# Performance work log

Measured on AMD Instinct MI355X. Metric: run time of the kernel, lower is better.

## Reference

```python
import jax, jax.numpy as jnp
import numpy as np

IN_DIM = 128
OUT_DIM = 128
NUM_INTERVALS = 8
SPLINE_ORDER = 3
BATCH = 1024


def make_grids():
    # domain [-1, 1] for every (in, out) pair, extended by spline_order knots each side
    step = 2.0 / NUM_INTERVALS
    G = NUM_INTERVALS + 2 * SPLINE_ORDER + 1
    g = (-1.0 - SPLINE_ORDER * step) + jnp.arange(G, dtype=jnp.float32) * step  # [G]
    return jnp.broadcast_to(g, (IN_DIM, OUT_DIM, G))


def setup_inputs() -> dict:
    key = jax.random.key(0)
    k1, k2, k3 = jax.random.split(key, 3)
    x = jax.random.normal(k1, (BATCH, IN_DIM), dtype=jnp.float32)
    n_cp = NUM_INTERVALS + SPLINE_ORDER
    control_points = 0.1 * jax.random.normal(k2, (IN_DIM, OUT_DIM, n_cp), dtype=jnp.float32)
    scaling_factors = np.sqrt(2.0 / OUT_DIM).astype(np.float32) * jax.random.normal(
        k3, (IN_DIM, OUT_DIM), dtype=jnp.float32)
    grids = make_grids()
    return {"x": x, "control_points": control_points,
            "scaling_factors": scaling_factors, "grids": grids}


def bspline_bases(x, grids, k):
    # Bottom-up Cox-de-Boor DP (identical recurrence to the naive top-down version).
    # x: [B, in], grids: [in, out, G] -> returns all degree-k bases [B, in, out, G-1-k]
    ex = x[:, :, None, None]          # [B, in, 1, 1]
    t = grids[None]                   # [1, in, out, G]
    B = ((t[..., :-1] <= ex) & (ex < t[..., 1:])).astype(x.dtype)  # degree 0
    for d in range(1, k + 1):
        tl  = t[..., : -(d + 1)]      # t[i]
        tr  = t[..., d:-1]            # t[i+d]
        tl1 = t[..., 1:-d]            # t[i+1]
        tr1 = t[..., d + 1:]          # t[i+d+1]
        B = (ex - tl) / (tr - tl) * B[..., :-1] + (tr1 - ex) / (tr1 - tl1) * B[..., 1:]
    return B


def reference(x, control_points, scaling_factors, grids):
    Bk = bspline_bases(x, grids, SPLINE_ORDER)                 # [B, in, out, n_cp]
    spline = jnp.einsum('biog,iog->bio', Bk, control_points)    # [B, in, out]
    res = scaling_factors[None] * (jax.nn.silu(x)[:, :, None] + spline)
    return jnp.sum(res, axis=1).astype(jnp.float32)             # [B, out]
```

## Files before the change

### kernel.cpp

```cpp
#include <hip/hip_runtime.h>
#include <math.h>


#define IN_DIM   128
#define OUT_DIM  128
#define NCP      11
#define GK       15
#define FS       12
#define KTOT     (IN_DIM * FS)
#define BT       8
#define OT       32
#define VO       4
#define KSP      32
#define NJ       12
#define THREADS  256
#define RPAD     260

__global__ __launch_bounds__(256)
void kan_prep(const float* __restrict__ CP,
              const float* __restrict__ SF,
              float* __restrict__ W)
{
    const int p = blockIdx.x * 256 + threadIdx.x;
    const int i = p >> 7;
    const int o = p & (OUT_DIM - 1);
    const float s = SF[p];
    const float* cp = CP + p * NCP;
    const int kb = i * FS;
    #pragma unroll
    for (int g = 0; g < NCP; ++g)
        W[(kb + g) * OUT_DIM + o] = s * cp[g];
    W[(kb + NCP) * OUT_DIM + o] = s;
}

__global__ __launch_bounds__(THREADS, 2)
void kan_main(const float* __restrict__ X,
              const float* __restrict__ GR,
              const float* __restrict__ W,
              float* __restrict__ OUT)
{
    __shared__ float F[BT * KTOT];

    const int tid = threadIdx.x;
    const int b0  = blockIdx.x * BT;
    const int o0  = blockIdx.y * OT;

    const float t0 = GR[0];
    const float h  = GR[1] - t0;
    const float r1 = 1.0f / h;
    const float r2 = 1.0f / (2.0f * h);
    const float r3 = 1.0f / (3.0f * h);
    float kn[GK];
    #pragma unroll
    for (int j = 0; j < GK; ++j) kn[j] = t0 + (float)j * h;

    #pragma unroll
    for (int kq = 0; kq < (BT * IN_DIM) / THREADS; ++kq) {
        const int p = tid + kq * THREADS;
        const int r = p >> 7;
        const int i = p & (IN_DIM - 1);

        const float x = X[(b0 + r) * IN_DIM + i];

        float b[GK - 1];
        #pragma unroll
        for (int j = 0; j < GK - 1; ++j)
            b[j] = (kn[j] <= x && x < kn[j + 1]) ? 1.0f : 0.0f;
        #pragma unroll
        for (int j = 0; j < GK - 2; ++j)
            b[j] = ((x - kn[j]) * b[j] + (kn[j + 2] - x) * b[j + 1]) * r1;
        #pragma unroll
        for (int j = 0; j < GK - 3; ++j)
            b[j] = ((x - kn[j]) * b[j] + (kn[j + 3] - x) * b[j + 1]) * r2;
        #pragma unroll
        for (int j = 0; j < GK - 4; ++j)
            b[j] = ((x - kn[j]) * b[j] + (kn[j + 4] - x) * b[j + 1]) * r3;

        const float silu = x / (1.0f + __expf(-x));

        float* f = &F[p * FS];
        *(float4*)(f + 0) = make_float4(b[0], b[1], b[2], b[3]);
        *(float4*)(f + 4) = make_float4(b[4], b[5], b[6], b[7]);
        *(float4*)(f + 8) = make_float4(b[8], b[9], b[10], silu);
    }
    __syncthreads();

    const int ol = tid & (OT / VO - 1);
    const int ks = tid >> 3;
    const int o4 = o0 + VO * ol;

    float acc[BT][VO];
    #pragma unroll
    for (int r = 0; r < BT; ++r)
        #pragma unroll
        for (int v = 0; v < VO; ++v) acc[r][v] = 0.0f;

    #pragma unroll
    for (int j = 0; j < NJ; ++j) {
        const int kg = 4 * (ks + KSP * j);

        float4 w0 = *(const float4*)&W[(kg + 0) * OUT_DIM + o4];
        float4 w1 = *(const float4*)&W[(kg + 1) * OUT_DIM + o4];
        float4 w2 = *(const float4*)&W[(kg + 2) * OUT_DIM + o4];
        float4 w3 = *(const float4*)&W[(kg + 3) * OUT_DIM + o4];

        #pragma unroll
        for (int r = 0; r < BT; ++r) {
            const float4 f = *(const float4*)&F[r * KTOT + kg];
            acc[r][0] = fmaf(f.x, w0.x, acc[r][0]);
            acc[r][1] = fmaf(f.x, w0.y, acc[r][1]);
            acc[r][2] = fmaf(f.x, w0.z, acc[r][2]);
            acc[r][3] = fmaf(f.x, w0.w, acc[r][3]);
            acc[r][0] = fmaf(f.y, w1.x, acc[r][0]);
            acc[r][1] = fmaf(f.y, w1.y, acc[r][1]);
            acc[r][2] = fmaf(f.y, w1.z, acc[r][2]);
            acc[r][3] = fmaf(f.y, w1.w, acc[r][3]);
            acc[r][0] = fmaf(f.z, w2.x, acc[r][0]);
            acc[r][1] = fmaf(f.z, w2.y, acc[r][1]);
            acc[r][2] = fmaf(f.z, w2.z, acc[r][2]);
            acc[r][3] = fmaf(f.z, w2.w, acc[r][3]);
            acc[r][0] = fmaf(f.w, w3.x, acc[r][0]);
            acc[r][1] = fmaf(f.w, w3.y, acc[r][1]);
            acc[r][2] = fmaf(f.w, w3.z, acc[r][2]);
            acc[r][3] = fmaf(f.w, w3.w, acc[r][3]);
        }
    }

    __syncthreads();
    float* red = F;
    #pragma unroll
    for (int r = 0; r < BT; ++r)
        *(float4*)&red[ks * RPAD + r * OT + VO * ol] =
            make_float4(acc[r][0], acc[r][1], acc[r][2], acc[r][3]);
    __syncthreads();

    {
        const int r  = tid >> 5;
        const int oc = tid & 31;
        float v = 0.0f;
        #pragma unroll
        for (int q = 0; q < KSP; ++q)
            v += red[q * RPAD + r * OT + oc];
        OUT[(b0 + r) * OUT_DIM + o0 + oc] = v;
    }
}

extern "C" void kernel_launch(void* const* d_in, const int* in_sizes, int n_in,
                              void* d_out, int out_size, void* d_ws, size_t ws_size,
                              hipStream_t stream) {
    const float* x  = (const float*)d_in[0];
    const float* cp = (const float*)d_in[1];
    const float* sf = (const float*)d_in[2];
    const float* gr = (const float*)d_in[3];
    float* out = (float*)d_out;
    float* W   = (float*)d_ws;

    const int batch = in_sizes[0] / IN_DIM;

    kan_prep<<<(IN_DIM * OUT_DIM) / 256, 256, 0, stream>>>(cp, sf, W);
    dim3 grid(batch / BT, OUT_DIM / OT);
    kan_main<<<grid, THREADS, 0, stream>>>(x, gr, W, out);
}
```

Baseline: 69.31 us.

## Fuse weight prep into main kernel, reading control points and scales directly

```diff
diff --git a/kernel.cpp b/kernel.cpp
--- a/kernel.cpp
+++ b/kernel.cpp
@@ -12,32 +12,23 @@
 #define OT       32
 #define VO       4
 #define KSP      32
-#define NJ       12
+#define NI       (IN_DIM / KSP)
 #define THREADS  256
 #define RPAD     260
 
-__global__ __launch_bounds__(256)
-void kan_prep(const float* __restrict__ CP,
-              const float* __restrict__ SF,
-              float* __restrict__ W)
-{
-    const int p = blockIdx.x * 256 + threadIdx.x;
-    const int i = p >> 7;
-    const int o = p & (OUT_DIM - 1);
-    const float s = SF[p];
-    const float* cp = CP + p * NCP;
-    const int kb = i * FS;
-    #pragma unroll
-    for (int g = 0; g < NCP; ++g)
-        W[(kb + g) * OUT_DIM + o] = s * cp[g];
-    W[(kb + NCP) * OUT_DIM + o] = s;
+typedef float f4v __attribute__((ext_vector_type(4)));
+typedef f4v uf4 __attribute__((aligned(4)));
+
+__device__ __forceinline__ f4v ld4u(const float* __restrict__ p) {
+    return *(const uf4*)p;
 }
 
 __global__ __launch_bounds__(THREADS, 2)
-void kan_main(const float* __restrict__ X,
-              const float* __restrict__ GR,
-              const float* __restrict__ W,
-              float* __restrict__ OUT)
+void kan_fused(const float* __restrict__ X,
+               const float* __restrict__ CP,
+               const float* __restrict__ SF,
+               const float* __restrict__ GR,
+               float* __restrict__ OUT)
 {
     __shared__ float F[BT * KTOT];
 
@@ -96,33 +87,51 @@
         for (int v = 0; v < VO; ++v) acc[r][v] = 0.0f;
 
     #pragma unroll
-    for (int j = 0; j < NJ; ++j) {
-        const int kg = 4 * (ks + KSP * j);
+    for (int jj = 0; jj < NI; ++jj) {
+        const int i = ks + KSP * jj;
+        const float4 sf4 = *(const float4*)&SF[i * OUT_DIM + o4];
+        const float* cb = CP + (i * OUT_DIM + o4) * NCP;
 
-        float4 w0 = *(const float4*)&W[(kg + 0) * OUT_DIM + o4];
-        float4 w1 = *(const float4*)&W[(kg + 1) * OUT_DIM + o4];
-        float4 w2 = *(const float4*)&W[(kg + 2) * OUT_DIM + o4];
-        float4 w3 = *(const float4*)&W[(kg + 3) * OUT_DIM + o4];
+        f4v c[VO][3];
+        #pragma unroll
+        for (int v = 0; v < VO; ++v) {
+            const float s = (v == 0) ? sf4.x : (v == 1) ? sf4.y
+                          : (v == 2) ? sf4.z : sf4.w;
+            const float* cv = cb + v * NCP;
+            f4v a0 = ld4u(cv + 0);
+            f4v a1 = ld4u(cv + 4);
+            f4v a2 = ld4u(cv + 7);
+            c[v][0] = s * a0;
+            c[v][1] = s * a1;
+            c[v][2].x = s;
+            c[v][2].y = s * a2.y;
+            c[v][2].z = s * a2.z;
+            c[v][2].w = s * a2.w;
+        }
 
+        const int fb = i * FS;
         #pragma unroll
         for (int r = 0; r < BT; ++r) {
-            const float4 f = *(const float4*)&F[r * KTOT + kg];
-            acc[r][0] = fmaf(f.x, w0.x, acc[r][0]);
-            acc[r][1] = fmaf(f.x, w0.y, acc[r][1]);
-            acc[r][2] = fmaf(f.x, w0.z, acc[r][2]);
-            acc[r][3] = fmaf(f.x, w0.w, acc[r][3]);
-            acc[r][0] = fmaf(f.y, w1.x, acc[r][0]);
-            acc[r][1] = fmaf(f.y, w1.y, acc[r][1]);
-            acc[r][2] = fmaf(f.y, w1.z, acc[r][2]);
-            acc[r][3] = fmaf(f.y, w1.w, acc[r][3]);
-            acc[r][0] = fmaf(f.z, w2.x, acc[r][0]);
-            acc[r][1] = fmaf(f.z, w2.y, acc[r][1]);
-            acc[r][2] = fmaf(f.z, w2.z, acc[r][2]);
-            acc[r][3] = fmaf(f.z, w2.w, acc[r][3]);
-            acc[r][0] = fmaf(f.w, w3.x, acc[r][0]);
-            acc[r][1] = fmaf(f.w, w3.y, acc[r][1]);
-            acc[r][2] = fmaf(f.w, w3.z, acc[r][2]);
-            acc[r][3] = fmaf(f.w, w3.w, acc[r][3]);
+            const float4 f0 = *(const float4*)&F[r * KTOT + fb + 0];
+            const float4 f1 = *(const float4*)&F[r * KTOT + fb + 4];
+            const float4 f2 = *(const float4*)&F[r * KTOT + fb + 8];
+            #pragma unroll
+            for (int v = 0; v < VO; ++v) {
+                float a = acc[r][v];
+                a = fmaf(f0.x, c[v][0].x, a);
+                a = fmaf(f0.y, c[v][0].y, a);
+                a = fmaf(f0.z, c[v][0].z, a);
+                a = fmaf(f0.w, c[v][0].w, a);
+                a = fmaf(f1.x, c[v][1].x, a);
+                a = fmaf(f1.y, c[v][1].y, a);
+                a = fmaf(f1.z, c[v][1].z, a);
+                a = fmaf(f1.w, c[v][1].w, a);
+                a = fmaf(f2.x, c[v][2].y, a);
+                a = fmaf(f2.y, c[v][2].z, a);
+                a = fmaf(f2.z, c[v][2].w, a);
+                a = fmaf(f2.w, c[v][2].x, a);
+                acc[r][v] = a;
+            }
         }
     }
 
@@ -153,11 +162,10 @@
     const float* sf = (const float*)d_in[2];
     const float* gr = (const float*)d_in[3];
     float* out = (float*)d_out;
-    float* W   = (float*)d_ws;
+    (void)d_ws; (void)ws_size;
 
     const int batch = in_sizes[0] / IN_DIM;
 
-    kan_prep<<<(IN_DIM * OUT_DIM) / 256, 256, 0, stream>>>(cp, sf, W);
     dim3 grid(batch / BT, OUT_DIM / OT);
-    kan_main<<<grid, THREADS, 0, stream>>>(x, gr, W, out);
+    kan_fused<<<grid, THREADS, 0, stream>>>(x, cp, sf, gr, out);
 }
```

Measured after the change: 78.07 us. 1.13x slower.
